# Performance work log

Measured on AMD Instinct MI355X. Metric: run time of the kernel, lower is better.

Reference implementation:

```python
import jax, jax.numpy as jnp
import numpy as np

# Daubechies-4 (db2) orthonormal filters (Dwork-style wtDaubechies2 coefficients)
_S3 = np.sqrt(3.0)
_DEN = 4.0 * np.sqrt(2.0)
_LO = np.array([1.0 + _S3, 3.0 + _S3, 3.0 - _S3, 1.0 - _S3], dtype=np.float32) / _DEN
_HI = np.array([1.0 - _S3, _S3 - 3.0, 3.0 + _S3, -(1.0 + _S3)], dtype=np.float32) / _DEN


def _up2(a, axis):
    """Upsample by 2 along `axis` (zeros at odd positions)."""
    a = jnp.moveaxis(a, axis, -1)
    u = jnp.stack([a, jnp.zeros_like(a)], axis=-1).reshape(*a.shape[:-1], 2 * a.shape[-1])
    return jnp.moveaxis(u, -1, axis)


def _cconv(u, f, axis):
    """Circular convolution y[n] = sum_k f[k] u[n-k] (filter length 4)."""
    return sum(float(f[k]) * jnp.roll(u, k, axis=axis) for k in range(len(f)))


def _ilevel(wt):
    """One level of separable 2D inverse db2 (periodized, orthonormal -> W^T)."""
    H, W = wt.shape
    # invert along rows (axis 0): low half on top, high half on bottom
    t = _cconv(_up2(wt[: H // 2], 0), _LO, 0) + _cconv(_up2(wt[H // 2 :], 0), _HI, 0)
    # invert along cols (axis 1)
    return _cconv(_up2(t[:, : W // 2], 1), _LO, 1) + _cconv(_up2(t[:, W // 2 :], 1), _HI, 1)


def _iwt2(wt, levels):
    if levels > 1:
        H, W = wt.shape
        sub = _iwt2(wt[: H // 2, : W // 2], levels - 1)
        wt = wt.at[: H // 2, : W // 2].set(sub)
    return _ilevel(wt)


def setup_inputs() -> dict:
    key = jax.random.key(0)
    k1, k2, k3 = jax.random.split(key, 3)
    N = 4096
    x = jax.random.normal(k1, (1, N, N), dtype=jnp.float32)
    mask = jax.random.uniform(k2, (N, N), dtype=jnp.float32)
    b = jax.random.normal(k3, (N, N), dtype=jnp.float32)
    wavSplit = jnp.ones((4, 4), dtype=jnp.int32)  # 4x4 split -> 3 levels
    return {"x": x, "mask": mask, "b": b, "wavSplit": wavSplit}


def reference(x, mask, b, wavSplit):
    # levels derived from the (static) split shape: 2^(L-1) == split side
    levels = int(np.log2(wavSplit.shape[0])) + 1
    return _iwt2(jnp.squeeze(x), levels)
```

## Files before the change

### kernel.cpp

```cpp
#include <hip/hip_runtime.h>

#define H_0 0.48296291314469025f
#define H_1 0.8365163037378079f
#define H_2 0.22414386804201336f
#define H_3 (-0.12940952255092145f)
#define G_0 (-0.12940952255092145f)
#define G_1 (-0.22414386804201336f)
#define G_2 0.8365163037378079f
#define G_3 (-0.48296291314469025f)


__device__ __forceinline__ float4 rowpass4(float h0, float h2, float g0, float g2,
                                           const float4& P, const float4& Q,
                                           const float4& R, const float4& T) {
    return make_float4(h0 * P.x + h2 * Q.x + g0 * R.x + g2 * T.x,
                       h0 * P.y + h2 * Q.y + g0 * R.y + g2 * T.y,
                       h0 * P.z + h2 * Q.z + g0 * R.z + g2 * T.z,
                       h0 * P.w + h2 * Q.w + g0 * R.w + g2 * T.w);
}

__device__ __forceinline__ void colpass_store(float* __restrict__ dst,
                                              const float4 L, const float Lm1,
                                              const float4 Hi, const float Hm1) {
    float4 s0, s1;
    s0.x = H_0 * L.x + H_2 * Lm1 + G_0 * Hi.x + G_2 * Hm1;
    s0.y = H_1 * L.x + H_3 * Lm1 + G_1 * Hi.x + G_3 * Hm1;
    s0.z = H_0 * L.y + H_2 * L.x + G_0 * Hi.y + G_2 * Hi.x;
    s0.w = H_1 * L.y + H_3 * L.x + G_1 * Hi.y + G_3 * Hi.x;
    s1.x = H_0 * L.z + H_2 * L.y + G_0 * Hi.z + G_2 * Hi.y;
    s1.y = H_1 * L.z + H_3 * L.y + G_1 * Hi.z + G_3 * Hi.y;
    s1.z = H_0 * L.w + H_2 * L.z + G_0 * Hi.w + G_2 * Hi.z;
    s1.w = H_1 * L.w + H_3 * L.z + G_1 * Hi.w + G_3 * Hi.z;
    *reinterpret_cast<float4*>(dst) = s0;
    *reinterpret_cast<float4*>(dst + 4) = s1;
}

template <int K>
__global__ __launch_bounds__(256) void iwt_roll(
    const float* __restrict__ x, int ldx,
    const float* __restrict__ sub, int ldsub,
    float* __restrict__ out, int ldo,
    int S2, int segShift) {
    const int lane = threadIdx.x & 63;
    const int wid = (blockIdx.x * 256 + threadIdx.x) >> 6;
    const int seg = wid & ((1 << segShift) - 1);
    const int m0 = (wid >> segShift) * K;
    const int cl = (seg << 8) + (lane << 2);
    const int cm1 = (cl == 0) ? (S2 - 1) : (cl - 1);

    const bool hasSub = (sub != nullptr);
    const float* __restrict__ pA = hasSub ? sub : x;
    const int ldA = hasSub ? ldsub : ldx;

    const int mp0 = (m0 == 0) ? (S2 - 1) : (m0 - 1);
    float4 Ap = *reinterpret_cast<const float4*>(pA + (size_t)mp0 * ldA + cl);
    float4 Bp = *reinterpret_cast<const float4*>(x + (size_t)(S2 + mp0) * ldx + cl);
    float4 Cp = *reinterpret_cast<const float4*>(x + (size_t)mp0 * ldx + S2 + cl);
    float4 Dp = *reinterpret_cast<const float4*>(x + (size_t)(S2 + mp0) * ldx + S2 + cl);
    float ap = pA[(size_t)mp0 * ldA + cm1];
    float bp = x[(size_t)(S2 + mp0) * ldx + cm1];
    float cp = x[(size_t)mp0 * ldx + S2 + cm1];
    float dp = x[(size_t)(S2 + mp0) * ldx + S2 + cm1];

#pragma unroll
    for (int i = 0; i < K; ++i) {
        const int m = m0 + i;
        const float4 A = *reinterpret_cast<const float4*>(pA + (size_t)m * ldA + cl);
        const float4 B = *reinterpret_cast<const float4*>(x + (size_t)(S2 + m) * ldx + cl);
        const float4 C = *reinterpret_cast<const float4*>(x + (size_t)m * ldx + S2 + cl);
        const float4 D = *reinterpret_cast<const float4*>(x + (size_t)(S2 + m) * ldx + S2 + cl);
        const float a = pA[(size_t)m * ldA + cm1];
        const float b = x[(size_t)(S2 + m) * ldx + cm1];
        const float c = x[(size_t)m * ldx + S2 + cm1];
        const float d = x[(size_t)(S2 + m) * ldx + S2 + cm1];

        const float4 TL0 = rowpass4(H_0, H_2, G_0, G_2, A, Ap, B, Bp);
        const float4 TL1 = rowpass4(H_1, H_3, G_1, G_3, A, Ap, B, Bp);
        const float4 TH0 = rowpass4(H_0, H_2, G_0, G_2, C, Cp, D, Dp);
        const float4 TH1 = rowpass4(H_1, H_3, G_1, G_3, C, Cp, D, Dp);

        const float mL0 = H_0 * a + H_2 * ap + G_0 * b + G_2 * bp;
        const float mL1 = H_1 * a + H_3 * ap + G_1 * b + G_3 * bp;
        const float mH0 = H_0 * c + H_2 * cp + G_0 * d + G_2 * dp;
        const float mH1 = H_1 * c + H_3 * cp + G_1 * d + G_3 * dp;

        float* o0 = out + (size_t)(2 * m) * ldo + 2 * cl;
        colpass_store(o0, TL0, mL0, TH0, mH0);
        colpass_store(o0 + ldo, TL1, mL1, TH1, mH1);

        Ap = A; Bp = B; Cp = C; Dp = D;
        ap = a; bp = b; cp = c; dp = d;
    }
}

extern "C" void kernel_launch(void* const* d_in, const int* in_sizes, int n_in,
                              void* d_out, int out_size, void* d_ws, size_t ws_size,
                              hipStream_t stream) {
    const float* x = (const float*)d_in[0];
    float* out = (float*)d_out;
    float* buf1 = (float*)d_ws;
    float* buf2 = (float*)((char*)d_ws + ((size_t)16 << 20));

    const int N = 4096;

    iwt_roll<1><<<256, 256, 0, stream>>>(x, N, nullptr, 0, buf1, 1024, 512, 1);
    iwt_roll<1><<<1024, 256, 0, stream>>>(x, N, buf1, 1024, buf2, 2048, 1024, 2);
    iwt_roll<4><<<1024, 256, 0, stream>>>(x, N, buf2, 2048, out, N, 2048, 3);
}
```

Measured before the change: 45.32 us.

## Stage row-pass results in shared memory per row strip before column pass

```diff
diff --git a/kernel.cpp b/kernel.cpp
--- a/kernel.cpp
+++ b/kernel.cpp
@@ -11,85 +11,91 @@
 
 
 __device__ __forceinline__ float4 rowpass4(float h0, float h2, float g0, float g2,
-                                           const float4& P, const float4& Q,
-                                           const float4& R, const float4& T) {
-    return make_float4(h0 * P.x + h2 * Q.x + g0 * R.x + g2 * T.x,
-                       h0 * P.y + h2 * Q.y + g0 * R.y + g2 * T.y,
-                       h0 * P.z + h2 * Q.z + g0 * R.z + g2 * T.z,
-                       h0 * P.w + h2 * Q.w + g0 * R.w + g2 * T.w);
+                                           const float4& P_, const float4& Q_,
+                                           const float4& R_, const float4& T_) {
+    return make_float4(h0 * P_.x + h2 * Q_.x + g0 * R_.x + g2 * T_.x,
+                       h0 * P_.y + h2 * Q_.y + g0 * R_.y + g2 * T_.y,
+                       h0 * P_.z + h2 * Q_.z + g0 * R_.z + g2 * T_.z,
+                       h0 * P_.w + h2 * Q_.w + g0 * R_.w + g2 * T_.w);
 }
 
-__device__ __forceinline__ void colpass_store(float* __restrict__ dst,
-                                              const float4 L, const float Lm1,
-                                              const float4 Hi, const float Hm1) {
-    float4 s0, s1;
-    s0.x = H_0 * L.x + H_2 * Lm1 + G_0 * Hi.x + G_2 * Hm1;
-    s0.y = H_1 * L.x + H_3 * Lm1 + G_1 * Hi.x + G_3 * Hm1;
-    s0.z = H_0 * L.y + H_2 * L.x + G_0 * Hi.y + G_2 * Hi.x;
-    s0.w = H_1 * L.y + H_3 * L.x + G_1 * Hi.y + G_3 * Hi.x;
-    s1.x = H_0 * L.z + H_2 * L.y + G_0 * Hi.z + G_2 * Hi.y;
-    s1.y = H_1 * L.z + H_3 * L.y + G_1 * Hi.z + G_3 * Hi.y;
-    s1.z = H_0 * L.w + H_2 * L.z + G_0 * Hi.w + G_2 * Hi.z;
-    s1.w = H_1 * L.w + H_3 * L.z + G_1 * Hi.w + G_3 * Hi.z;
-    *reinterpret_cast<float4*>(dst) = s0;
-    *reinterpret_cast<float4*>(dst + 4) = s1;
-}
-
-template <int K>
-__global__ __launch_bounds__(256) void iwt_roll(
+template <int S2, int P, int T>
+__global__ __launch_bounds__(T, 8) void iwt_strip(
     const float* __restrict__ x, int ldx,
     const float* __restrict__ sub, int ldsub,
-    float* __restrict__ out, int ldo,
-    int S2, int segShift) {
-    const int lane = threadIdx.x & 63;
-    const int wid = (blockIdx.x * 256 + threadIdx.x) >> 6;
-    const int seg = wid & ((1 << segShift) - 1);
-    const int m0 = (wid >> segShift) * K;
-    const int cl = (seg << 8) + (lane << 2);
-    const int cm1 = (cl == 0) ? (S2 - 1) : (cl - 1);
+    float* __restrict__ out, int ldo) {
+    constexpr int S = 2 * S2;
+    constexpr int Q = S2 / 4;
+    constexpr int RT = P * S2 / 2;
+    constexpr int ITER = RT / T;
 
+    __shared__ float tl[P][2][S];
+
+    const int tid = threadIdx.x;
+    const int m0 = blockIdx.x * P;
     const bool hasSub = (sub != nullptr);
     const float* __restrict__ pA = hasSub ? sub : x;
     const int ldA = hasSub ? ldsub : ldx;
 
-    const int mp0 = (m0 == 0) ? (S2 - 1) : (m0 - 1);
-    float4 Ap = *reinterpret_cast<const float4*>(pA + (size_t)mp0 * ldA + cl);
-    float4 Bp = *reinterpret_cast<const float4*>(x + (size_t)(S2 + mp0) * ldx + cl);
-    float4 Cp = *reinterpret_cast<const float4*>(x + (size_t)mp0 * ldx + S2 + cl);
-    float4 Dp = *reinterpret_cast<const float4*>(x + (size_t)(S2 + mp0) * ldx + S2 + cl);
-    float ap = pA[(size_t)mp0 * ldA + cm1];
-    float bp = x[(size_t)(S2 + mp0) * ldx + cm1];
-    float cp = x[(size_t)mp0 * ldx + S2 + cm1];
-    float dp = x[(size_t)(S2 + mp0) * ldx + S2 + cm1];
+#pragma unroll
+    for (int k = 0; k < ITER; ++k) {
+        const int rt = tid + k * T;
+        const int q = rt % Q;
+        const int half = (rt / Q) % 2;
+        const int p = rt / (2 * Q);
+        const int m = m0 + p;
+        const int mp = (m == 0) ? (S2 - 1) : (m - 1);
+        const int cb = 4 * q;
+        const int xcb = half ? (S2 + cb) : cb;
+
+        float4 A, Apv;
+        if (half == 0) {
+            A   = *reinterpret_cast<const float4*>(pA + (size_t)m  * ldA + cb);
+            Apv = *reinterpret_cast<const float4*>(pA + (size_t)mp * ldA + cb);
+        } else {
+            A   = *reinterpret_cast<const float4*>(x + (size_t)m  * ldx + xcb);
+            Apv = *reinterpret_cast<const float4*>(x + (size_t)mp * ldx + xcb);
+        }
+        const float4 B  = *reinterpret_cast<const float4*>(x + (size_t)(S2 + m)  * ldx + xcb);
+        const float4 Bp = *reinterpret_cast<const float4*>(x + (size_t)(S2 + mp) * ldx + xcb);
+
+        const float4 t0 = rowpass4(H_0, H_2, G_0, G_2, A, Apv, B, Bp);
+        const float4 t1 = rowpass4(H_1, H_3, G_1, G_3, A, Apv, B, Bp);
+        *reinterpret_cast<float4*>(&tl[p][0][xcb]) = t0;
+        *reinterpret_cast<float4*>(&tl[p][1][xcb]) = t1;
+    }
+    __syncthreads();
 
 #pragma unroll
-    for (int i = 0; i < K; ++i) {
-        const int m = m0 + i;
-        const float4 A = *reinterpret_cast<const float4*>(pA + (size_t)m * ldA + cl);
-        const float4 B = *reinterpret_cast<const float4*>(x + (size_t)(S2 + m) * ldx + cl);
-        const float4 C = *reinterpret_cast<const float4*>(x + (size_t)m * ldx + S2 + cl);
-        const float4 D = *reinterpret_cast<const float4*>(x + (size_t)(S2 + m) * ldx + S2 + cl);
-        const float a = pA[(size_t)m * ldA + cm1];
-        const float b = x[(size_t)(S2 + m) * ldx + cm1];
-        const float c = x[(size_t)m * ldx + S2 + cm1];
-        const float d = x[(size_t)(S2 + m) * ldx + S2 + cm1];
+    for (int k = 0; k < ITER; ++k) {
+        const int ct = tid + k * T;
+        const int cg = ct % Q;
+        const int r2 = ct / Q;
+        const int p = r2 >> 1;
+        const int orr = r2 & 1;
+        const int n0 = 4 * cg;
+        const int np = (n0 == 0) ? (S2 - 4) : (n0 - 4);
 
-        const float4 TL0 = rowpass4(H_0, H_2, G_0, G_2, A, Ap, B, Bp);
-        const float4 TL1 = rowpass4(H_1, H_3, G_1, G_3, A, Ap, B, Bp);
-        const float4 TH0 = rowpass4(H_0, H_2, G_0, G_2, C, Cp, D, Dp);
-        const float4 TH1 = rowpass4(H_1, H_3, G_1, G_3, C, Cp, D, Dp);
+        const float* trow = tl[p][orr];
+        const float4 L  = *reinterpret_cast<const float4*>(&trow[n0]);
+        const float4 Lp = *reinterpret_cast<const float4*>(&trow[np]);
+        const float4 Hi = *reinterpret_cast<const float4*>(&trow[S2 + n0]);
+        const float4 Hp = *reinterpret_cast<const float4*>(&trow[S2 + np]);
+        const float Lm1 = Lp.w, Hm1 = Hp.w;
 
-        const float mL0 = H_0 * a + H_2 * ap + G_0 * b + G_2 * bp;
-        const float mL1 = H_1 * a + H_3 * ap + G_1 * b + G_3 * bp;
-        const float mH0 = H_0 * c + H_2 * cp + G_0 * d + G_2 * dp;
-        const float mH1 = H_1 * c + H_3 * cp + G_1 * d + G_3 * dp;
+        float4 s0, s1;
+        s0.x = H_0 * L.x + H_2 * Lm1 + G_0 * Hi.x + G_2 * Hm1;
+        s0.y = H_1 * L.x + H_3 * Lm1 + G_1 * Hi.x + G_3 * Hm1;
+        s0.z = H_0 * L.y + H_2 * L.x + G_0 * Hi.y + G_2 * Hi.x;
+        s0.w = H_1 * L.y + H_3 * L.x + G_1 * Hi.y + G_3 * Hi.x;
+        s1.x = H_0 * L.z + H_2 * L.y + G_0 * Hi.z + G_2 * Hi.y;
+        s1.y = H_1 * L.z + H_3 * L.y + G_1 * Hi.z + G_3 * Hi.y;
+        s1.z = H_0 * L.w + H_2 * L.z + G_0 * Hi.w + G_2 * Hi.z;
+        s1.w = H_1 * L.w + H_3 * L.z + G_1 * Hi.w + G_3 * Hi.z;
 
-        float* o0 = out + (size_t)(2 * m) * ldo + 2 * cl;
-        colpass_store(o0, TL0, mL0, TH0, mH0);
-        colpass_store(o0 + ldo, TL1, mL1, TH1, mH1);
-
-        Ap = A; Bp = B; Cp = C; Dp = D;
-        ap = a; bp = b; cp = c; dp = d;
+        float* o = out + (size_t)(2 * (m0 + p) + orr) * ldo + 8 * cg;
+        *reinterpret_cast<float4*>(o) = s0;
+        *reinterpret_cast<float4*>(o + 4) = s1;
     }
 }
 
@@ -103,7 +109,7 @@
 
     const int N = 4096;
 
-    iwt_roll<1><<<256, 256, 0, stream>>>(x, N, nullptr, 0, buf1, 1024, 512, 1);
-    iwt_roll<1><<<1024, 256, 0, stream>>>(x, N, buf1, 1024, buf2, 2048, 1024, 2);
-    iwt_roll<4><<<1024, 256, 0, stream>>>(x, N, buf2, 2048, out, N, 2048, 3);
+    iwt_strip<512, 4, 512><<<128, 512, 0, stream>>>(x, N, nullptr, 0, buf1, 1024);
+    iwt_strip<1024, 4, 1024><<<256, 1024, 0, stream>>>(x, N, buf1, 1024, buf2, 2048);
+    iwt_strip<2048, 2, 1024><<<1024, 1024, 0, stream>>>(x, N, buf2, 2048, out, N);
 }
```

New measurement: 45.22 us. About the same (-0.2%).
